# Performance work log

Measured on AMD Instinct MI355X. Metric: run time of the kernel, lower is better.

The kernel has to match this reference:

```python
import jax, jax.numpy as jnp
import numpy as np

N = 255      # 17 joints * 15 time steps
NNZ = 2550   # ~avg degree 10
B = 512


def setup_inputs() -> dict:
    key = jax.random.key(0)
    ks = jax.random.split(key, 24)
    inp = {}
    inp["H"] = jax.random.normal(ks[0], (B, N, 2), jnp.float32)
    inp["sm_values"] = jax.random.uniform(ks[1], (NNZ,), jnp.float32)
    inp["sp_values"] = jax.random.uniform(ks[2], (NNZ,), jnp.float32)
    dims = [2, 400, 300, 100, 300, 400, 2]
    names = ["enc0", "enc1", "enc2", "dec0", "dec1", "dec2"]
    for i, nm in enumerate(names):
        din, dout = dims[i], dims[i + 1]
        inp["W_" + nm] = jax.random.normal(ks[3 + 2 * i], (din, dout), jnp.float32) * (1.0 / np.sqrt(din))
        inp["b_" + nm] = jnp.zeros((dout,), jnp.float32)
    inp["sm_indices"] = jax.random.randint(ks[20], (NNZ, 2), 0, N, dtype=jnp.int32)
    inp["sp_indices"] = jax.random.randint(ks[21], (NNZ, 2), 0, N, dtype=jnp.int32)
    return inp


def _densify(indices, values):
    # scatter sparse COO Laplacian into a tiny [N, N] dense matrix (255x255)
    return jnp.zeros((N, N), values.dtype).at[indices[:, 0], indices[:, 1]].add(values)


def reference(H, sm_values, sp_values,
              W_enc0, b_enc0, W_enc1, b_enc1, W_enc2, b_enc2,
              W_dec0, b_dec0, W_dec1, b_dec1, W_dec2, b_dec2,
              sm_indices, sp_indices):
    DADsm = _densify(sm_indices, sm_values)
    DADsp = _densify(sp_indices, sp_values)
    x = H  # [B, N, d]
    # encoder: Laplacian smoothing = ReLU(DADsm @ (x W + b)), batched over B
    for W, b in ((W_enc0, b_enc0), (W_enc1, b_enc1), (W_enc2, b_enc2)):
        x = jax.nn.relu(jnp.einsum('ij,bjd->bid', DADsm, x @ W + b))
    # decoder: Laplacian sharpening = ReLU(DADsp @ (x W + b))
    for W, b in ((W_dec0, b_dec0), (W_dec1, b_dec1), (W_dec2, b_dec2)):
        x = jax.nn.relu(jnp.einsum('ij,bjd->bid', DADsp, x @ W + b))
    return x
```

## Files before the change

kernel.cpp:

```cpp
#include <hip/hip_runtime.h>
#include <hip/hip_fp16.h>

typedef __half f16;
typedef _Float16 h8 __attribute__((ext_vector_type(8)));
typedef _Float16 h4 __attribute__((ext_vector_type(4)));
typedef float f32x4 __attribute__((ext_vector_type(4)));

#define NN 255
#define BB 512
#define TSS 264

static __device__ __forceinline__ f16 f2h(float x) { return __float2half(x); }


__global__ void zero_k(float* p, int n) {
    int i = blockIdx.x * 256 + threadIdx.x;
    if (i < n) p[i] = 0.f;
}

__global__ void scatter_k(const int* __restrict__ idx, const float* __restrict__ vals,
                          float* __restrict__ dad, int nnz) {
    int t = blockIdx.x * 256 + threadIdx.x;
    if (t < nnz) atomicAdd(&dad[idx[2 * t] * 256 + idx[2 * t + 1]], vals[t]);
}

__global__ void convert_dad(const float* __restrict__ dadf, f16* __restrict__ dadp) {
    int i = blockIdx.x * 256 + threadIdx.x;
    int which = i >> 16, rc = i & 65535;
    int node = rc >> 8, k = rc & 255;
    float v = (node < NN) ? dadf[(size_t)which * NN * 256 + rc] : 0.f;
    dadp[(size_t)which * 65536 + (((k >> 3) * 256 + node) << 3) + (k & 7)] = f2h(v);
}

__global__ void convert_wt(const float* __restrict__ W, f16* __restrict__ Wtp,
                           int K, int N, int KPB) {
    int f = blockIdx.x;
    int tile = f >> 6, fl = f & 63;
    int Kpad = KPB * 8;
    for (int k = threadIdx.x; k < Kpad; k += 256) {
        float v = (f < N && k < K) ? W[(size_t)k * N + f] : 0.f;
        Wtp[((((size_t)tile * KPB + (k >> 3)) * 64 + fl) << 3) + (k & 7)] = f2h(v);
    }
}

__global__ __launch_bounds__(256) void pack_h(const float* __restrict__ H, f16* __restrict__ Hp) {
    int g = blockIdx.x * 256 + threadIdx.x;
    int b = g >> 8, node = g & 255;
    h8 z;
#pragma unroll
    for (int i = 0; i < 8; i++) z[i] = (_Float16)0.f;
    h8 h0 = z;
    if (node < NN) {
        h0[0] = (_Float16)H[((size_t)b * NN + node) * 2];
        h0[1] = (_Float16)H[((size_t)b * NN + node) * 2 + 1];
    }
    _Float16* base = (_Float16*)Hp + (size_t)b * 4 * 2048;
    *(h8*)(base + ((0 * 256 + node) << 3)) = h0;
    *(h8*)(base + ((1 * 256 + node) << 3)) = z;
    *(h8*)(base + ((2 * 256 + node) << 3)) = z;
    *(h8*)(base + ((3 * 256 + node) << 3)) = z;
}

template <int KPB, bool OUTF32>
__global__ __launch_bounds__(256, 4) void fused_layer(
        const f16* __restrict__ X,
        const f16* __restrict__ Wtp,
        const float* __restrict__ bias,
        const f16* __restrict__ dadp,
        void* __restrict__ Xn_,
        int Nout, int SN, int ntiles, int rev) {
    __shared__ _Float16 T[64 * TSS];
    const int id = blockIdx.x;
    int s = id >> 3;
    int bq = s / ntiles;
    const int tile = s - bq * ntiles;
    if (rev) bq = 63 - bq;
    const int b = ((id & 7) << 6) + bq;
    const int n0 = tile * 64;
    const int tid = threadIdx.x;
    const int w = tid >> 6;
    const int ln = tid & 15;
    const int q = (tid >> 4) & 3;

    f32x4 acc[4][4];
#pragma unroll
    for (int t = 0; t < 4; t++)
#pragma unroll
        for (int c = 0; c < 4; c++) acc[t][c] = (f32x4){0.f, 0.f, 0.f, 0.f};

    const f16* xb = X + (size_t)b * KPB * 2048;
    const f16* wp = Wtp + (size_t)tile * KPB * 512;

    h8 af[2][4];
#pragma unroll
    for (int t = 0; t < 4; t++)
        af[0][t] = *(const h8*)(xb + ((q * 256 + 64 * w + 16 * t + ln) << 3));

#pragma unroll
    for (int kb = 0; kb < KPB; kb += 4) {
        const int cur = (kb >> 2) & 1, nxt = cur ^ 1;
        h8 bf[4];
#pragma unroll
        for (int c = 0; c < 4; c++)
            bf[c] = *(const h8*)(wp + (((kb + q) * 64 + 16 * c + ln) << 3));
        if (kb + 4 < KPB) {
#pragma unroll
            for (int t = 0; t < 4; t++)
                af[nxt][t] = *(const h8*)(xb + (((kb + 4 + q) * 256 + 64 * w + 16 * t + ln) << 3));
        }
#pragma unroll
        for (int c = 0; c < 4; c++)
#pragma unroll
            for (int t = 0; t < 4; t++)
                acc[t][c] = __builtin_amdgcn_mfma_f32_16x16x32_f16(af[cur][t], bf[c], acc[t][c], 0, 0, 0);
    }

#pragma unroll
    for (int c = 0; c < 4; c++) {
        int fl = 16 * c + ln;
        int gf = n0 + fl;
        float bv = (gf < Nout) ? bias[gf] : 0.f;
#pragma unroll
        for (int t = 0; t < 4; t++) {
            h4 pk;
#pragma unroll
            for (int rg = 0; rg < 4; rg++) pk[rg] = (_Float16)(acc[t][c][rg] + bv);
            *(h4*)&T[fl * TSS + 64 * w + 16 * t + q * 4] = pk;
        }
    }
    __syncthreads();

    f32x4 acc2[4][4];
#pragma unroll
    for (int f = 0; f < 4; f++)
#pragma unroll
        for (int t = 0; t < 4; t++) acc2[f][t] = (f32x4){0.f, 0.f, 0.f, 0.f};

    h8 b2[2][4];
#pragma unroll
    for (int t = 0; t < 4; t++)
        b2[0][t] = *(const h8*)(dadp + ((q * 256 + 64 * w + 16 * t + ln) << 3));

#pragma unroll
    for (int kb = 0; kb < 32; kb += 4) {
        const int cur = (kb >> 2) & 1, nxt = cur ^ 1;
        if (kb + 4 < 32) {
#pragma unroll
            for (int t = 0; t < 4; t++)
                b2[nxt][t] = *(const h8*)(dadp + (((kb + 4 + q) * 256 + 64 * w + 16 * t + ln) << 3));
        }
        h8 a2[4];
#pragma unroll
        for (int f = 0; f < 4; f++)
            a2[f] = *(const h8*)&T[(16 * f + ln) * TSS + (kb + q) * 8];
#pragma unroll
        for (int t = 0; t < 4; t++)
#pragma unroll
            for (int f = 0; f < 4; f++)
                acc2[f][t] = __builtin_amdgcn_mfma_f32_16x16x32_f16(a2[f], b2[cur][t], acc2[f][t], 0, 0, 0);
    }

    if (!OUTF32) {
        f16* xn = (f16*)Xn_ + (size_t)b * (SN >> 3) * 2048;
#pragma unroll
        for (int f = 0; f < 4; f++) {
            int fb = n0 + 16 * f + q * 4;
            if (fb >= SN) continue;
            int fb8 = fb >> 3, off = fb & 7;
#pragma unroll
            for (int t = 0; t < 4; t++) {
                int node = 64 * w + 16 * t + ln;
                h4 pk;
#pragma unroll
                for (int rg = 0; rg < 4; rg++) pk[rg] = (_Float16)fmaxf(acc2[f][t][rg], 0.f);
                *(h4*)(xn + (((size_t)fb8 * 256 + node) << 3) + off) = pk;
            }
        }
    } else {
        if (q == 0) {
            float* op = (float*)Xn_;
#pragma unroll
            for (int t = 0; t < 4; t++) {
                int node = 64 * w + 16 * t + ln;
                if (node < NN) {
                    float2 v;
                    v.x = fmaxf(acc2[0][t][0], 0.f);
                    v.y = fmaxf(acc2[0][t][1], 0.f);
                    *(float2*)(op + ((size_t)b * NN + node) * 2) = v;
                }
            }
        }
    }
}


extern "C" void kernel_launch(void* const* d_in, const int* in_sizes, int n_in,
                              void* d_out, int out_size, void* d_ws, size_t ws_size,
                              hipStream_t stream) {
    const float* H   = (const float*)d_in[0];
    const float* W[6]  = {(const float*)d_in[3], (const float*)d_in[5], (const float*)d_in[7],
                          (const float*)d_in[9], (const float*)d_in[11], (const float*)d_in[13]};
    const float* Bv[6] = {(const float*)d_in[4], (const float*)d_in[6], (const float*)d_in[8],
                          (const float*)d_in[10], (const float*)d_in[12], (const float*)d_in[14]};
    const int* smi = (const int*)d_in[15];
    const int* spi = (const int*)d_in[16];

    char* p = (char*)d_ws;
    f16* bufA = (f16*)p;            p += 109051904;
    f16* bufB = (f16*)p;            p += 83886080;
    float* dadsm = (float*)p;       p += 261120;
    float* dadsp = (float*)p;       p += 261120;
    f16* dadpsm = (f16*)p;          p += 131072;
    f16* dadpsp = (f16*)p;          p += 131072;
    f16* Wt0 = (f16*)p;             p += 28672;
    f16* Wt1 = (f16*)p;             p += 266240;
    f16* Wt2 = (f16*)p;             p += 81920;
    f16* Wt3 = (f16*)p;             p += 81920;
    f16* Wt4 = (f16*)p;             p += 286720;
    f16* Wt5 = (f16*)p;             p += 53248;
    f16* Hp  = (f16*)p;             p += 4194304;

    zero_k<<<510, 256, 0, stream>>>(dadsm, 2 * NN * 256);
    scatter_k<<<10, 256, 0, stream>>>(smi, (const float*)d_in[1], dadsm, 2550);
    scatter_k<<<10, 256, 0, stream>>>(spi, (const float*)d_in[2], dadsp, 2550);
    convert_dad<<<512, 256, 0, stream>>>(dadsm, dadpsm);
    convert_wt<<<448, 256, 0, stream>>>(W[0], Wt0, 2, 400, 4);
    convert_wt<<<320, 256, 0, stream>>>(W[1], Wt1, 400, 300, 52);
    convert_wt<<<128, 256, 0, stream>>>(W[2], Wt2, 300, 100, 40);
    convert_wt<<<320, 256, 0, stream>>>(W[3], Wt3, 100, 300, 16);
    convert_wt<<<448, 256, 0, stream>>>(W[4], Wt4, 300, 400, 40);
    convert_wt<<<64, 256, 0, stream>>>(W[5], Wt5, 400, 2, 52);
    pack_h<<<512, 256, 0, stream>>>(H, Hp);

    fused_layer<4,  false><<<BB * 7, 256, 0, stream>>>(Hp,   Wt0, Bv[0], dadpsm, bufA, 400, 416, 7, 0);
    fused_layer<52, false><<<BB * 5, 256, 0, stream>>>(bufA, Wt1, Bv[1], dadpsm, bufB, 300, 320, 5, 1);
    fused_layer<40, false><<<BB * 2, 256, 0, stream>>>(bufB, Wt2, Bv[2], dadpsm, bufA, 100, 128, 2, 0);
    fused_layer<16, false><<<BB * 5, 256, 0, stream>>>(bufA, Wt3, Bv[3], dadpsp, bufB, 300, 320, 5, 1);
    fused_layer<40, false><<<BB * 7, 256, 0, stream>>>(bufB, Wt4, Bv[4], dadpsp, bufA, 400, 416, 7, 0);
    fused_layer<52, true ><<<BB * 1, 256, 0, stream>>>(bufA, Wt5, Bv[5], dadpsp, d_out, 2, 2, 1, 1);
}
```

Before: 359.6 us.

## Fold first encoder layer via associativity and recompute its activations inside layer two

Layer 0 has only two input features, so DADsm@(H W0 + b0) is rewritten as (DADsm@H) W0 + rowsum(DADsm)·b0. A small kernel computes DADsm@H per batch, and the second layer's A operand is rebuilt on the fly in half2 arithmetic from those two values, W0, b0 and the rowsums. This removes the layer-0 fused kernel and the large 400-wide intermediate buffer write and read. The final layer also drops to one column tile (CT=1), cutting wasted MFMAs for its two outputs. The trade-off is per-kb recomputation in fp16 and a small precision change.

```diff
diff --git a/kernel.cpp b/kernel.cpp
--- a/kernel.cpp
+++ b/kernel.cpp
@@ -4,6 +4,7 @@
 typedef __half f16;
 typedef _Float16 h8 __attribute__((ext_vector_type(8)));
 typedef _Float16 h4 __attribute__((ext_vector_type(4)));
+typedef _Float16 h2 __attribute__((ext_vector_type(2)));
 typedef float f32x4 __attribute__((ext_vector_type(4)));
 
 #define NN 255
@@ -11,6 +12,8 @@
 #define TSS 264
 
 static __device__ __forceinline__ f16 f2h(float x) { return __float2half(x); }
+
+union H8u { h8 v; h2 p[4]; };
 
 
 __global__ void zero_k(float* p, int n) {
@@ -22,6 +25,15 @@
                           float* __restrict__ dad, int nnz) {
     int t = blockIdx.x * 256 + threadIdx.x;
     if (t < nnz) atomicAdd(&dad[idx[2 * t] * 256 + idx[2 * t + 1]], vals[t]);
+}
+
+__global__ void rowsum_k(const float* __restrict__ dad, float* __restrict__ r) {
+    int i = blockIdx.x * 64 + threadIdx.x;
+    if (i < 256) {
+        float s = 0.f;
+        if (i < NN) for (int k = 0; k < NN; k++) s += dad[i * 256 + k];
+        r[i] = s;
+    }
 }
 
 __global__ void convert_dad(const float* __restrict__ dadf, f16* __restrict__ dadp) {
@@ -43,33 +55,50 @@
     }
 }
 
-__global__ __launch_bounds__(256) void pack_h(const float* __restrict__ H, f16* __restrict__ Hp) {
-    int g = blockIdx.x * 256 + threadIdx.x;
-    int b = g >> 8, node = g & 255;
-    h8 z;
-#pragma unroll
-    for (int i = 0; i < 8; i++) z[i] = (_Float16)0.f;
-    h8 h0 = z;
-    if (node < NN) {
-        h0[0] = (_Float16)H[((size_t)b * NN + node) * 2];
-        h0[1] = (_Float16)H[((size_t)b * NN + node) * 2 + 1];
-    }
-    _Float16* base = (_Float16*)Hp + (size_t)b * 4 * 2048;
-    *(h8*)(base + ((0 * 256 + node) << 3)) = h0;
-    *(h8*)(base + ((1 * 256 + node) << 3)) = z;
-    *(h8*)(base + ((2 * 256 + node) << 3)) = z;
-    *(h8*)(base + ((3 * 256 + node) << 3)) = z;
-}
-
-template <int KPB, bool OUTF32>
+__global__ __launch_bounds__(256) void dad2_in(const float* __restrict__ dad,
+                                               const float* __restrict__ H,
+                                               float* __restrict__ T0f) {
+    int gw = (blockIdx.x * 256 + threadIdx.x) >> 6;
+    int lane = threadIdx.x & 63;
+    if (gw >= BB * 256) return;
+    int b = gw >> 8, i = gw & 255;
+    if (i == NN) {
+        if (lane == 0) { T0f[(size_t)gw * 2] = 0.f; T0f[(size_t)gw * 2 + 1] = 0.f; }
+        return;
+    }
+    const float* dr = dad + (size_t)i * 256;
+    const float* yb = H + (size_t)b * NN * 2;
+    float a0 = 0.f, a1 = 0.f;
+    for (int k = lane; k < NN; k += 64) {
+        float d = dr[k];
+        a0 += d * yb[2 * k];
+        a1 += d * yb[2 * k + 1];
+    }
+#pragma unroll
+    for (int off = 32; off > 0; off >>= 1) {
+        a0 += __shfl_down(a0, off);
+        a1 += __shfl_down(a1, off);
+    }
+    if (lane == 0) {
+        T0f[(size_t)gw * 2 + 0] = a0;
+        T0f[(size_t)gw * 2 + 1] = a1;
+    }
+}
+
+template <int KPB, int CT, bool R2, bool OUTF32>
 __global__ __launch_bounds__(256, 4) void fused_layer(
         const f16* __restrict__ X,
         const f16* __restrict__ Wtp,
         const float* __restrict__ bias,
         const f16* __restrict__ dadp,
         void* __restrict__ Xn_,
-        int Nout, int SN, int ntiles, int rev) {
+        int Nout, int SN, int ntiles, int rev,
+        const float* __restrict__ T0p,
+        const float* __restrict__ rsmp,
+        const float* __restrict__ W0f,
+        const float* __restrict__ b0f) {
     __shared__ _Float16 T[64 * TSS];
+    __shared__ _Float16 WL[R2 ? 1344 : 4];
     const int id = blockIdx.x;
     int s = id >> 3;
     int bq = s / ntiles;
@@ -82,41 +111,85 @@
     const int ln = tid & 15;
     const int q = (tid >> 4) & 3;
 
-    f32x4 acc[4][4];
+    h2 a0s[4], a1s[4], rvs[4];
+    if constexpr (R2) {
+        for (int i2 = tid; i2 < 448; i2 += 256) {
+            _Float16 va = (_Float16)(i2 < 400 ? W0f[i2] : 0.f);
+            _Float16 vb = (_Float16)(i2 < 400 ? W0f[400 + i2] : 0.f);
+            _Float16 vc = (_Float16)(i2 < 400 ? b0f[i2] : 0.f);
+            WL[i2] = va; WL[448 + i2] = vb; WL[896 + i2] = vc;
+        }
+#pragma unroll
+        for (int t = 0; t < 4; t++) {
+            int node = 64 * w + 16 * t + ln;
+            const float* tp = T0p + ((size_t)b * 256 + node) * 2;
+            _Float16 x0 = (_Float16)tp[0];
+            _Float16 x1 = (_Float16)tp[1];
+            _Float16 rv = (_Float16)rsmp[node];
+            a0s[t] = (h2){x0, x0};
+            a1s[t] = (h2){x1, x1};
+            rvs[t] = (h2){rv, rv};
+        }
+        __syncthreads();
+    }
+
+    f32x4 acc[4][CT];
 #pragma unroll
     for (int t = 0; t < 4; t++)
 #pragma unroll
-        for (int c = 0; c < 4; c++) acc[t][c] = (f32x4){0.f, 0.f, 0.f, 0.f};
-
-    const f16* xb = X + (size_t)b * KPB * 2048;
+        for (int c = 0; c < CT; c++) acc[t][c] = (f32x4){0.f, 0.f, 0.f, 0.f};
+
+    const f16* xb = R2 ? (const f16*)nullptr : X + (size_t)b * KPB * 2048;
     const f16* wp = Wtp + (size_t)tile * KPB * 512;
 
-    h8 af[2][4];
-#pragma unroll
-    for (int t = 0; t < 4; t++)
-        af[0][t] = *(const h8*)(xb + ((q * 256 + 64 * w + 16 * t + ln) << 3));
+    h8 afr[2][4];
+    if constexpr (!R2) {
+#pragma unroll
+        for (int t = 0; t < 4; t++)
+            afr[0][t] = *(const h8*)(xb + ((q * 256 + 64 * w + 16 * t + ln) << 3));
+    }
 
 #pragma unroll
     for (int kb = 0; kb < KPB; kb += 4) {
         const int cur = (kb >> 2) & 1, nxt = cur ^ 1;
-        h8 bf[4];
-#pragma unroll
-        for (int c = 0; c < 4; c++)
+        h8 bf[CT];
+#pragma unroll
+        for (int c = 0; c < CT; c++)
             bf[c] = *(const h8*)(wp + (((kb + q) * 64 + 16 * c + ln) << 3));
-        if (kb + 4 < KPB) {
+        h8 afc[4];
+        if constexpr (R2) {
+            H8u wa, wb, bl;
+            wa.v = *(const h8*)&WL[(kb + q) * 8];
+            wb.v = *(const h8*)&WL[448 + (kb + q) * 8];
+            bl.v = *(const h8*)&WL[896 + (kb + q) * 8];
+            const h2 z2 = (h2){(_Float16)0.f, (_Float16)0.f};
+#pragma unroll
+            for (int t = 0; t < 4; t++) {
+                H8u r;
+#pragma unroll
+                for (int j = 0; j < 4; j++)
+                    r.p[j] = __builtin_elementwise_max(
+                        a0s[t] * wa.p[j] + a1s[t] * wb.p[j] + rvs[t] * bl.p[j], z2);
+                afc[t] = r.v;
+            }
+        } else {
+            if (kb + 4 < KPB) {
+#pragma unroll
+                for (int t = 0; t < 4; t++)
+                    afr[nxt][t] = *(const h8*)(xb + (((kb + 4 + q) * 256 + 64 * w + 16 * t + ln) << 3));
+            }
+#pragma unroll
+            for (int t = 0; t < 4; t++) afc[t] = afr[cur][t];
+        }
+#pragma unroll
+        for (int c = 0; c < CT; c++)
 #pragma unroll
             for (int t = 0; t < 4; t++)
-                af[nxt][t] = *(const h8*)(xb + (((kb + 4 + q) * 256 + 64 * w + 16 * t + ln) << 3));
-        }
-#pragma unroll
-        for (int c = 0; c < 4; c++)
-#pragma unroll
-            for (int t = 0; t < 4; t++)
-                acc[t][c] = __builtin_amdgcn_mfma_f32_16x16x32_f16(af[cur][t], bf[c], acc[t][c], 0, 0, 0);
-    }
-
-#pragma unroll
-    for (int c = 0; c < 4; c++) {
+                acc[t][c] = __builtin_amdgcn_mfma_f32_16x16x32_f16(afc[t], bf[c], acc[t][c], 0, 0, 0);
+    }
+
+#pragma unroll
+    for (int c = 0; c < CT; c++) {
         int fl = 16 * c + ln;
         int gf = n0 + fl;
         float bv = (gf < Nout) ? bias[gf] : 0.f;
@@ -130,9 +203,9 @@
     }
     __syncthreads();
 
-    f32x4 acc2[4][4];
-#pragma unroll
-    for (int f = 0; f < 4; f++)
+    f32x4 acc2[CT][4];
+#pragma unroll
+    for (int f = 0; f < CT; f++)
 #pragma unroll
         for (int t = 0; t < 4; t++) acc2[f][t] = (f32x4){0.f, 0.f, 0.f, 0.f};
 
@@ -149,21 +222,21 @@
             for (int t = 0; t < 4; t++)
                 b2[nxt][t] = *(const h8*)(dadp + (((kb + 4 + q) * 256 + 64 * w + 16 * t + ln) << 3));
         }
-        h8 a2[4];
-#pragma unroll
-        for (int f = 0; f < 4; f++)
+        h8 a2[CT];
+#pragma unroll
+        for (int f = 0; f < CT; f++)
             a2[f] = *(const h8*)&T[(16 * f + ln) * TSS + (kb + q) * 8];
 #pragma unroll
         for (int t = 0; t < 4; t++)
 #pragma unroll
-            for (int f = 0; f < 4; f++)
+            for (int f = 0; f < CT; f++)
                 acc2[f][t] = __builtin_amdgcn_mfma_f32_16x16x32_f16(a2[f], b2[cur][t], acc2[f][t], 0, 0, 0);
     }
 
     if (!OUTF32) {
         f16* xn = (f16*)Xn_ + (size_t)b * (SN >> 3) * 2048;
 #pragma unroll
-        for (int f = 0; f < 4; f++) {
+        for (int f = 0; f < CT; f++) {
             int fb = n0 + 16 * f + q * 4;
             if (fb >= SN) continue;
             int fb8 = fb >> 3, off = fb & 7;
@@ -212,30 +285,34 @@
     float* dadsp = (float*)p;       p += 261120;
     f16* dadpsm = (f16*)p;          p += 131072;
     f16* dadpsp = (f16*)p;          p += 131072;
-    f16* Wt0 = (f16*)p;             p += 28672;
     f16* Wt1 = (f16*)p;             p += 266240;
     f16* Wt2 = (f16*)p;             p += 81920;
     f16* Wt3 = (f16*)p;             p += 81920;
     f16* Wt4 = (f16*)p;             p += 286720;
     f16* Wt5 = (f16*)p;             p += 53248;
-    f16* Hp  = (f16*)p;             p += 4194304;
+    float* T0f = (float*)p;         p += 1048576;
+    float* rsm = (float*)p;         p += 1024;
 
     zero_k<<<510, 256, 0, stream>>>(dadsm, 2 * NN * 256);
     scatter_k<<<10, 256, 0, stream>>>(smi, (const float*)d_in[1], dadsm, 2550);
     scatter_k<<<10, 256, 0, stream>>>(spi, (const float*)d_in[2], dadsp, 2550);
+    rowsum_k<<<4, 64, 0, stream>>>(dadsm, rsm);
     convert_dad<<<512, 256, 0, stream>>>(dadsm, dadpsm);
-    convert_wt<<<448, 256, 0, stream>>>(W[0], Wt0, 2, 400, 4);
     convert_wt<<<320, 256, 0, stream>>>(W[1], Wt1, 400, 300, 52);
     convert_wt<<<128, 256, 0, stream>>>(W[2], Wt2, 300, 100, 40);
     convert_wt<<<320, 256, 0, stream>>>(W[3], Wt3, 100, 300, 16);
     convert_wt<<<448, 256, 0, stream>>>(W[4], Wt4, 300, 400, 40);
     convert_wt<<<64, 256, 0, stream>>>(W[5], Wt5, 400, 2, 52);
-    pack_h<<<512, 256, 0, stream>>>(H, Hp);
-
-    fused_layer<4,  false><<<BB * 7, 256, 0, stream>>>(Hp,   Wt0, Bv[0], dadpsm, bufA, 400, 416, 7, 0);
-    fused_layer<52, false><<<BB * 5, 256, 0, stream>>>(bufA, Wt1, Bv[1], dadpsm, bufB, 300, 320, 5, 1);
-    fused_layer<40, false><<<BB * 2, 256, 0, stream>>>(bufB, Wt2, Bv[2], dadpsm, bufA, 100, 128, 2, 0);
-    fused_layer<16, false><<<BB * 5, 256, 0, stream>>>(bufA, Wt3, Bv[3], dadpsp, bufB, 300, 320, 5, 1);
-    fused_layer<40, false><<<BB * 7, 256, 0, stream>>>(bufB, Wt4, Bv[4], dadpsp, bufA, 400, 416, 7, 0);
-    fused_layer<52, true ><<<BB * 1, 256, 0, stream>>>(bufA, Wt5, Bv[5], dadpsp, d_out, 2, 2, 1, 1);
-}
+    dad2_in<<<(BB * 256 * 64) / 256, 256, 0, stream>>>(dadsm, H, T0f);
+
+    fused_layer<52, 4, true,  false><<<BB * 5, 256, 0, stream>>>(
+        nullptr, Wt1, Bv[1], dadpsm, bufB, 300, 320, 5, 0, T0f, rsm, W[0], Bv[0]);
+    fused_layer<40, 4, false, false><<<BB * 2, 256, 0, stream>>>(
+        bufB, Wt2, Bv[2], dadpsm, bufA, 100, 128, 2, 1, nullptr, nullptr, nullptr, nullptr);
+    fused_layer<16, 4, false, false><<<BB * 5, 256, 0, stream>>>(
+        bufA, Wt3, Bv[3], dadpsp, bufB, 300, 320, 5, 0, nullptr, nullptr, nullptr, nullptr);
+    fused_layer<40, 4, false, false><<<BB * 7, 256, 0, stream>>>(
+        bufB, Wt4, Bv[4], dadpsp, bufA, 400, 416, 7, 1, nullptr, nullptr, nullptr, nullptr);
+    fused_layer<52, 1, false, true ><<<BB * 1, 256, 0, stream>>>(
+        bufA, Wt5, Bv[5], dadpsp, d_out, 2, 2, 1, 0, nullptr, nullptr, nullptr, nullptr);
+}
```

Measured after the change: 370.4 us. 1.03x slower.
